# Kernel optimization log

Measured on AMD Instinct MI355X. Metric: run time of the kernel, lower is better.

## Reference

```python
import jax, jax.numpy as jnp
import numpy as np

T, B, V, H = 2048, 32, 512, 512


def setup_inputs() -> dict:
    key = jax.random.key(0)
    ks = jax.random.split(key, 7)
    s = 1.0 / np.sqrt(V + H)  # torch nn.Linear default init bound
    u = lambda k, shape: jax.random.uniform(k, shape, jnp.float32, -s, s)
    return {
        "inputs": jax.random.normal(ks[0], (T, B, V), jnp.float32),
        "state": jnp.zeros((1, B, H), jnp.float32),
        "W_reset": u(ks[1], (V + H, H)),
        "b_reset": u(ks[2], (H,)),
        "W_net": u(ks[3], (V + H, H)),
        "b_net": u(ks[4], (H,)),
        "W_update": u(ks[5], (V + H, H)),
        "b_update": u(ks[6], (H,)),
    }


def reference(inputs, state, W_reset, b_reset, W_net, b_net, W_update, b_update):
    # inputs: [T, B, V], state: [1, B, H]
    h0 = state[0]  # [B, H]

    def step(h, x):
        # x: [B, V], h: [B, H]
        xh = jnp.concatenate([x, h], axis=-1)               # [B, V+H]
        R = jax.nn.sigmoid(xh @ W_reset + b_reset)          # [B, H]
        xr = jnp.concatenate([x, h * R], axis=-1)           # [B, V+H]
        H_t = jnp.tanh(xr @ W_net + b_net)                  # candidate
        Z = jax.nn.sigmoid(xr @ W_update + b_update)        # NOTE: from (x, h*R), faithful to source
        h_new = Z * h + (1.0 - Z) * H_t
        return h_new, h_new

    h_final, states = jax.lax.scan(step, h0, inputs)        # states: [T, B, H]
    return states, h_final[None]                            # ([T,B,H], [1,B,H])
```

## Files before the change

kernel.cpp:

```cpp
#include <hip/hip_runtime.h>
#include <cstdint>
#include <cstddef>

#define T_STEPS 2048
#define BATCH   32
#define VDIM    512
#define HDIM    512
#define SLICES  8
#define COLS    64
#define KPT     64

typedef _Float16 half2v __attribute__((ext_vector_type(2)));
typedef _Float16 half8v __attribute__((ext_vector_type(8)));

__device__ __forceinline__ float dot2h(half2v a, half2v b, float c) {
#if __has_builtin(__builtin_amdgcn_fdot2)
    return __builtin_amdgcn_fdot2(a, b, c, false);
#else
    return fmaf((float)a.x, (float)b.x, fmaf((float)a.y, (float)b.y, c));
#endif
}

__device__ __forceinline__ unsigned long long loadt(const unsigned long long* p) {
    return __hip_atomic_load(p, __ATOMIC_RELAXED, __HIP_MEMORY_SCOPE_AGENT);
}
__device__ __forceinline__ void storet(unsigned long long* p, float v, unsigned tag) {
    unsigned long long x = ((unsigned long long)tag << 32) | (unsigned)__float_as_uint(v);
    __hip_atomic_store(p, x, __ATOMIC_RELAXED, __HIP_MEMORY_SCOPE_AGENT);
}

__global__ __launch_bounds__(256)
void xproj_gemm(const float* __restrict__ X,
                const float* __restrict__ W0, const float* __restrict__ b0,
                const float* __restrict__ W1, const float* __restrict__ b1,
                const float* __restrict__ W2, const float* __restrict__ b2,
                float* __restrict__ xp, int M)
{
    const int g = blockIdx.z;
    const float* W    = (g == 0) ? W0 : (g == 1) ? W1 : W2;
    const float* bias = (g == 0) ? b0 : (g == 1) ? b1 : b2;
    float* out = xp + (size_t)g * M * HDIM;

    __shared__ float As[16][68];
    __shared__ float Bs[16][64];

    const int tid = threadIdx.x;
    const int tx = tid & 15;
    const int ty = tid >> 4;
    const int row0 = blockIdx.y * 64;
    const int n0   = blockIdx.x * 64;

    const int lm = tid >> 2;
    const int lk = (tid & 3) * 4;
    const int bk = tid >> 4;
    const int bn = (tid & 15) * 4;

    float acc[4][4] = {};

    for (int k0 = 0; k0 < VDIM; k0 += 16) {
        float4 av = *(const float4*)&X[(size_t)(row0 + lm) * VDIM + k0 + lk];
        float4 bv = *(const float4*)&W[(size_t)(k0 + bk) * HDIM + n0 + bn];
        __syncthreads();
        As[lk + 0][lm] = av.x;
        As[lk + 1][lm] = av.y;
        As[lk + 2][lm] = av.z;
        As[lk + 3][lm] = av.w;
        *(float4*)&Bs[bk][bn] = bv;
        __syncthreads();
        #pragma unroll
        for (int kk = 0; kk < 16; ++kk) {
            float4 a = *(const float4*)&As[kk][ty * 4];
            float4 b = *(const float4*)&Bs[kk][tx * 4];
            float ar[4] = {a.x, a.y, a.z, a.w};
            float br[4] = {b.x, b.y, b.z, b.w};
            #pragma unroll
            for (int i = 0; i < 4; ++i)
                #pragma unroll
                for (int j = 0; j < 4; ++j)
                    acc[i][j] += ar[i] * br[j];
        }
    }

    float4 bb = *(const float4*)&bias[n0 + tx * 4];
    #pragma unroll
    for (int i = 0; i < 4; ++i) {
        const int row = row0 + ty * 4 + i;
        float4 o;
        o.x = acc[i][0] + bb.x;
        o.y = acc[i][1] + bb.y;
        o.z = acc[i][2] + bb.z;
        o.w = acc[i][3] + bb.w;
        *(float4*)&out[(size_t)row * HDIM + n0 + tx * 4] = o;
    }
}

__global__ __launch_bounds__(512)
__attribute__((amdgpu_waves_per_eu(2, 2)))
void gru_scan3(const float* __restrict__ xp,
               const float* __restrict__ Wrh, const float* __restrict__ Wnh,
               const float* __restrict__ Wzh,
               const float* __restrict__ state, float* __restrict__ out,
               unsigned long long* __restrict__ hT,
               unsigned long long* __restrict__ uT,
               int t0, int nt, int M)
{
    const int b   = blockIdx.x & (BATCH - 1);
    const int s   = blockIdx.x >> 5;
    const int tid = threadIdx.x;
    const int c   = tid & (COLS - 1);
    const int j   = tid >> 6;
    const int n   = s * COLS + c;

    __shared__ __align__(16) _Float16 hlds[HDIM];
    __shared__ __align__(16) _Float16 ulds[HDIM];
    __shared__ float redR[SLICES][COLS];
    __shared__ float redN[SLICES][COLS];
    __shared__ float redZ[SLICES][COLS];

    half2v w2r[KPT / 2], w2n[KPT / 2], w2z[KPT / 2];
    {
        const size_t coloff = (size_t)s * COLS + c;
        const float* pr = Wrh + (size_t)j * KPT * HDIM + coloff;
        const float* pn = Wnh + (size_t)j * KPT * HDIM + coloff;
        const float* pz = Wzh + (size_t)j * KPT * HDIM + coloff;
        #pragma unroll
        for (int q = 0; q < KPT / 2; ++q) {
            half2v r, nn, z;
            r.x  = (_Float16)pr[(size_t)(2 * q) * HDIM];
            r.y  = (_Float16)pr[(size_t)(2 * q + 1) * HDIM];
            nn.x = (_Float16)pn[(size_t)(2 * q) * HDIM];
            nn.y = (_Float16)pn[(size_t)(2 * q + 1) * HDIM];
            z.x  = (_Float16)pz[(size_t)(2 * q) * HDIM];
            z.y  = (_Float16)pz[(size_t)(2 * q + 1) * HDIM];
            w2r[q] = r; w2n[q] = nn; w2z[q] = z;
        }
        #pragma unroll
        for (int q = 0; q < KPT / 2; ++q)
            asm volatile("" : "+v"(w2r[q]), "+v"(w2n[q]), "+v"(w2z[q]));
    }

    const size_t bb32 = (size_t)b * HDIM;
    unsigned long long* hTb = hT + bb32;
    unsigned long long* uTb = uT + bb32;
    const size_t gs = (size_t)M * HDIM;

    for (int tt = 0; tt < nt; ++tt) {
        const int t = t0 + tt;

        float xr = 0.f, xnn = 0.f, xz = 0.f;
        const size_t rb = ((size_t)tt * BATCH + b) * HDIM;
        if (tid < COLS) {
            xr  = xp[rb + n];
            xnn = xp[gs + rb + n];
            xz  = xp[2 * gs + rb + n];
        }

        float hv, hcv = 0.f;
        if (t == 0) {
            hv = state[bb32 + tid];
            if (tid < COLS) hcv = state[bb32 + n];
        } else {
            unsigned long long v;
            do { v = loadt(hTb + tid); } while ((unsigned)(v >> 32) != (unsigned)t);
            hv = __uint_as_float((unsigned)v);
            if (tid < COLS) {
                do { v = loadt(hTb + n); } while ((unsigned)(v >> 32) != (unsigned)t);
                hcv = __uint_as_float((unsigned)v);
            }
        }

        hlds[tid] = (_Float16)hv;
        asm volatile("s_waitcnt lgkmcnt(0)" ::: "memory");
        __builtin_amdgcn_sched_barrier(0);

        {
            float aR = 0.f;
            const half8v* hp = (const half8v*)&hlds[j * KPT];
            #pragma unroll
            for (int q = 0; q < KPT / 8; ++q) {
                half8v h8 = hp[q];
                half2v p0 = {h8[0], h8[1]}, p1 = {h8[2], h8[3]};
                half2v p2 = {h8[4], h8[5]}, p3 = {h8[6], h8[7]};
                aR = dot2h(p0, w2r[4 * q + 0], aR);
                aR = dot2h(p1, w2r[4 * q + 1], aR);
                aR = dot2h(p2, w2r[4 * q + 2], aR);
                aR = dot2h(p3, w2r[4 * q + 3], aR);
            }
            redR[j][c] = aR;
        }
        __syncthreads();

        if (tid < COLS) {
            float sR = 0.f;
            #pragma unroll
            for (int jj = 0; jj < SLICES; ++jj) sR += redR[jj][c];
            float R = 1.f / (1.f + __expf(-(xr + sR)));
            storet(uTb + n, hcv * R, (unsigned)(t + 1));
        }

        {
            unsigned long long v;
            do { v = loadt(uTb + tid); } while ((unsigned)(v >> 32) != (unsigned)(t + 1));
            ulds[tid] = (_Float16)__uint_as_float((unsigned)v);
        }
        asm volatile("s_waitcnt lgkmcnt(0)" ::: "memory");
        __builtin_amdgcn_sched_barrier(0);

        {
            float aN = 0.f, aZ = 0.f;
            const half8v* up = (const half8v*)&ulds[j * KPT];
            #pragma unroll
            for (int q = 0; q < KPT / 8; ++q) {
                half8v u8 = up[q];
                half2v p0 = {u8[0], u8[1]}, p1 = {u8[2], u8[3]};
                half2v p2 = {u8[4], u8[5]}, p3 = {u8[6], u8[7]};
                aN = dot2h(p0, w2n[4 * q + 0], aN);
                aZ = dot2h(p0, w2z[4 * q + 0], aZ);
                aN = dot2h(p1, w2n[4 * q + 1], aN);
                aZ = dot2h(p1, w2z[4 * q + 1], aZ);
                aN = dot2h(p2, w2n[4 * q + 2], aN);
                aZ = dot2h(p2, w2z[4 * q + 2], aZ);
                aN = dot2h(p3, w2n[4 * q + 3], aN);
                aZ = dot2h(p3, w2z[4 * q + 3], aZ);
            }
            redN[j][c] = aN;
            redZ[j][c] = aZ;
        }
        __syncthreads();

        if (tid < COLS) {
            float sN = 0.f, sZ = 0.f;
            #pragma unroll
            for (int jj = 0; jj < SLICES; ++jj) { sN += redN[jj][c]; sZ += redZ[jj][c]; }
            float e  = __expf(2.f * (xnn + sN));
            float Hc = 1.f - 2.f / (e + 1.f);
            float Z  = 1.f / (1.f + __expf(-(xz + sZ)));
            float hnew = Z * hcv + (1.f - Z) * Hc;
            __builtin_nontemporal_store(hnew, out + (size_t)t * BATCH * HDIM + bb32 + n);
            storet(hTb + n, hnew, (unsigned)(t + 1));
            if (t == T_STEPS - 1)
                out[(size_t)T_STEPS * BATCH * HDIM + bb32 + n] = hnew;
        }
    }
}

extern "C" void kernel_launch(void* const* d_in, const int* in_sizes, int n_in,
                              void* d_out, int out_size, void* d_ws, size_t ws_size,
                              hipStream_t stream) {
    const float* inputs   = (const float*)d_in[0];
    const float* state    = (const float*)d_in[1];
    const float* W_reset  = (const float*)d_in[2];
    const float* b_reset  = (const float*)d_in[3];
    const float* W_net    = (const float*)d_in[4];
    const float* b_net    = (const float*)d_in[5];
    const float* W_update = (const float*)d_in[6];
    const float* b_update = (const float*)d_in[7];
    float* out = (float*)d_out;

    const size_t tail_bytes = 2ull * BATCH * HDIM * 8;
    size_t tail_base = (ws_size - tail_bytes) & ~(size_t)255;
    char* base = (char*)d_ws;
    float* xp = (float*)base;
    unsigned long long* hT = (unsigned long long*)(base + tail_base);
    unsigned long long* uT = hT + (size_t)BATCH * HDIM;

    const size_t per_t = 3ull * BATCH * HDIM * sizeof(float);
    int C = (int)(tail_base / per_t);
    if (C > T_STEPS) C = T_STEPS;
    C &= ~1;
    if (C < 2) C = 2;

    hipMemsetAsync(hT, 0xFF, tail_bytes, stream);

    for (int t0 = 0; t0 < T_STEPS; t0 += C) {
        const int nt = (T_STEPS - t0 < C) ? (T_STEPS - t0) : C;
        const int M  = nt * BATCH;

        dim3 g1(HDIM / 64, M / 64, 3);
        xproj_gemm<<<g1, 256, 0, stream>>>(inputs + (size_t)t0 * BATCH * VDIM,
                                           W_reset, b_reset,
                                           W_net,   b_net,
                                           W_update, b_update,
                                           xp, M);

        gru_scan3<<<BATCH * SLICES, 512, 0, stream>>>(
            xp,
            W_reset  + (size_t)VDIM * HDIM,
            W_net    + (size_t)VDIM * HDIM,
            W_update + (size_t)VDIM * HDIM,
            state, out, hT, uT, t0, nt, M);
    }
}
```

Before: 6.490 ms.

## Add fast sc0 flag path with slow atomic fallback for cross-block handoff

The tagged h and u values are now published twice: once with a raw sc0 global store into a 'fast' buffer and once with the agent-scope atomic store into a 'slow' buffer. Pollers read the fast buffer twice with inline-asm sc0 loads before falling back to the atomic load. The goal is lower latency for the per-step inter-workgroup handoff, which bounds the sequential recurrence. The owned column's h (hcv) is also kept in a register across steps instead of being re-polled each step, and the h publish is moved ahead of the output store. In exchange, visibility of the fast path depends on cache-coherence behaviour of sc0 on MI355X, every publish issues an extra store, and the workspace tail doubles in size.

Result: slower. 7.297 ms (+12.4%).

```diff
diff --git a/kernel.cpp b/kernel.cpp
--- a/kernel.cpp
+++ b/kernel.cpp
@@ -24,9 +24,33 @@
 __device__ __forceinline__ unsigned long long loadt(const unsigned long long* p) {
     return __hip_atomic_load(p, __ATOMIC_RELAXED, __HIP_MEMORY_SCOPE_AGENT);
 }
-__device__ __forceinline__ void storet(unsigned long long* p, float v, unsigned tag) {
+__device__ __forceinline__ unsigned long long fload(const unsigned long long* p) {
+    unsigned long long r;
+    asm volatile("global_load_dwordx2 %0, %1, off sc0\n\ts_waitcnt vmcnt(0)"
+                 : "=v"(r) : "v"(p) : "memory");
+    return r;
+}
+__device__ __forceinline__ void fstore(unsigned long long* p, unsigned long long x) {
+    asm volatile("global_store_dwordx2 %0, %1, off sc0" :: "v"(p), "v"(x) : "memory");
+}
+
+__device__ __forceinline__ void publish(unsigned long long* fast, unsigned long long* slow,
+                                        float v, unsigned tag) {
     unsigned long long x = ((unsigned long long)tag << 32) | (unsigned)__float_as_uint(v);
-    __hip_atomic_store(p, x, __ATOMIC_RELAXED, __HIP_MEMORY_SCOPE_AGENT);
+    fstore(fast, x);
+    __hip_atomic_store(slow, x, __ATOMIC_RELAXED, __HIP_MEMORY_SCOPE_AGENT);
+}
+
+__device__ __forceinline__ float poll_tag(const unsigned long long* fast,
+                                          const unsigned long long* slow, unsigned want) {
+    for (;;) {
+        unsigned long long v = fload(fast);
+        if ((unsigned)(v >> 32) == want) return __uint_as_float((unsigned)v);
+        v = fload(fast);
+        if ((unsigned)(v >> 32) == want) return __uint_as_float((unsigned)v);
+        v = loadt(slow);
+        if ((unsigned)(v >> 32) == want) return __uint_as_float((unsigned)v);
+    }
 }
 
 __global__ __launch_bounds__(256)
@@ -96,12 +120,12 @@
 
 __global__ __launch_bounds__(512)
 __attribute__((amdgpu_waves_per_eu(2, 2)))
-void gru_scan3(const float* __restrict__ xp,
+void gru_scan4(const float* __restrict__ xp,
                const float* __restrict__ Wrh, const float* __restrict__ Wnh,
                const float* __restrict__ Wzh,
                const float* __restrict__ state, float* __restrict__ out,
-               unsigned long long* __restrict__ hT,
-               unsigned long long* __restrict__ uT,
+               unsigned long long* __restrict__ hS, unsigned long long* __restrict__ uS,
+               unsigned long long* __restrict__ hF, unsigned long long* __restrict__ uF,
                int t0, int nt, int M)
 {
     const int b   = blockIdx.x & (BATCH - 1);
@@ -140,9 +164,13 @@
     }
 
     const size_t bb32 = (size_t)b * HDIM;
-    unsigned long long* hTb = hT + bb32;
-    unsigned long long* uTb = uT + bb32;
+    unsigned long long* hSb = hS + bb32;
+    unsigned long long* uSb = uS + bb32;
+    unsigned long long* hFb = hF + bb32;
+    unsigned long long* uFb = uF + bb32;
     const size_t gs = (size_t)M * HDIM;
+
+    float hcv = 0.f;
 
     for (int tt = 0; tt < nt; ++tt) {
         const int t = t0 + tt;
@@ -155,18 +183,14 @@
             xz  = xp[2 * gs + rb + n];
         }
 
-        float hv, hcv = 0.f;
+        float hv;
         if (t == 0) {
             hv = state[bb32 + tid];
             if (tid < COLS) hcv = state[bb32 + n];
         } else {
-            unsigned long long v;
-            do { v = loadt(hTb + tid); } while ((unsigned)(v >> 32) != (unsigned)t);
-            hv = __uint_as_float((unsigned)v);
-            if (tid < COLS) {
-                do { v = loadt(hTb + n); } while ((unsigned)(v >> 32) != (unsigned)t);
-                hcv = __uint_as_float((unsigned)v);
-            }
+            hv = poll_tag(hFb + tid, hSb + tid, (unsigned)t);
+            if (tt == 0 && tid < COLS)
+                hcv = poll_tag(hFb + n, hSb + n, (unsigned)t);
         }
 
         hlds[tid] = (_Float16)hv;
@@ -195,14 +219,10 @@
             #pragma unroll
             for (int jj = 0; jj < SLICES; ++jj) sR += redR[jj][c];
             float R = 1.f / (1.f + __expf(-(xr + sR)));
-            storet(uTb + n, hcv * R, (unsigned)(t + 1));
-        }
-
-        {
-            unsigned long long v;
-            do { v = loadt(uTb + tid); } while ((unsigned)(v >> 32) != (unsigned)(t + 1));
-            ulds[tid] = (_Float16)__uint_as_float((unsigned)v);
-        }
+            publish(uFb + n, uSb + n, hcv * R, (unsigned)(t + 1));
+        }
+
+        ulds[tid] = (_Float16)poll_tag(uFb + tid, uSb + tid, (unsigned)(t + 1));
         asm volatile("s_waitcnt lgkmcnt(0)" ::: "memory");
         __builtin_amdgcn_sched_barrier(0);
 
@@ -236,8 +256,9 @@
             float Hc = 1.f - 2.f / (e + 1.f);
             float Z  = 1.f / (1.f + __expf(-(xz + sZ)));
             float hnew = Z * hcv + (1.f - Z) * Hc;
+            publish(hFb + n, hSb + n, hnew, (unsigned)(t + 1));
             __builtin_nontemporal_store(hnew, out + (size_t)t * BATCH * HDIM + bb32 + n);
-            storet(hTb + n, hnew, (unsigned)(t + 1));
+            hcv = hnew;
             if (t == T_STEPS - 1)
                 out[(size_t)T_STEPS * BATCH * HDIM + bb32 + n] = hnew;
         }
@@ -257,12 +278,15 @@
     const float* b_update = (const float*)d_in[7];
     float* out = (float*)d_out;
 
-    const size_t tail_bytes = 2ull * BATCH * HDIM * 8;
+    const size_t buf_elems = (size_t)BATCH * HDIM;
+    const size_t tail_bytes = 4ull * buf_elems * 8;
     size_t tail_base = (ws_size - tail_bytes) & ~(size_t)255;
     char* base = (char*)d_ws;
     float* xp = (float*)base;
-    unsigned long long* hT = (unsigned long long*)(base + tail_base);
-    unsigned long long* uT = hT + (size_t)BATCH * HDIM;
+    unsigned long long* hS = (unsigned long long*)(base + tail_base);
+    unsigned long long* uS = hS + buf_elems;
+    unsigned long long* hF = uS + buf_elems;
+    unsigned long long* uF = hF + buf_elems;
 
     const size_t per_t = 3ull * BATCH * HDIM * sizeof(float);
     int C = (int)(tail_base / per_t);
@@ -270,7 +294,7 @@
     C &= ~1;
     if (C < 2) C = 2;
 
-    hipMemsetAsync(hT, 0xFF, tail_bytes, stream);
+    hipMemsetAsync(hS, 0xFF, tail_bytes, stream);
 
     for (int t0 = 0; t0 < T_STEPS; t0 += C) {
         const int nt = (T_STEPS - t0 < C) ? (T_STEPS - t0) : C;
@@ -283,11 +307,11 @@
                                            W_update, b_update,
                                            xp, M);
 
-        gru_scan3<<<BATCH * SLICES, 512, 0, stream>>>(
+        gru_scan4<<<BATCH * SLICES, 512, 0, stream>>>(
             xp,
             W_reset  + (size_t)VDIM * HDIM,
             W_net    + (size_t)VDIM * HDIM,
             W_update + (size_t)VDIM * HDIM,
-            state, out, hT, uT, t0, nt, M);
-    }
-}
+            state, out, hS, uS, hF, uF, t0, nt, M);
+    }
+}
```

## Repartition recurrent GEMVs by K-slice and exchange tagged partial sums instead of h

Applied to the files above, without the earlier changes.

The N and Z weight matrices are now split by input rows: each block owns a 64-row slice of h*R and computes partial sums for all 512 output columns. Each block keeps the full hidden state locally and exchanges tagged partial-sum packets (N in fp32, Z in fp16) through double-buffered global slots. This removes the cross-block h broadcast and the u exchange, leaving one global exchange per step instead of two. The cost is that every block redundantly computes the full h update, and each thread now polls eight global slots every step. Z partials are rounded to fp16 before being summed.

Measured after the change: 7.870 ms. 21.3% more time.

```diff
diff --git a/kernel.cpp b/kernel.cpp
--- a/kernel.cpp
+++ b/kernel.cpp
@@ -8,7 +8,6 @@
 #define HDIM    512
 #define SLICES  8
 #define COLS    64
-#define KPT     64
 
 typedef _Float16 half2v __attribute__((ext_vector_type(2)));
 typedef _Float16 half8v __attribute__((ext_vector_type(8)));
@@ -24,8 +23,7 @@
 __device__ __forceinline__ unsigned long long loadt(const unsigned long long* p) {
     return __hip_atomic_load(p, __ATOMIC_RELAXED, __HIP_MEMORY_SCOPE_AGENT);
 }
-__device__ __forceinline__ void storet(unsigned long long* p, float v, unsigned tag) {
-    unsigned long long x = ((unsigned long long)tag << 32) | (unsigned)__float_as_uint(v);
+__device__ __forceinline__ void storet(unsigned long long* p, unsigned long long x) {
     __hip_atomic_store(p, x, __ATOMIC_RELAXED, __HIP_MEMORY_SCOPE_AGENT);
 }
 
@@ -96,12 +94,12 @@
 
 __global__ __launch_bounds__(512)
 __attribute__((amdgpu_waves_per_eu(2, 2)))
-void gru_scan3(const float* __restrict__ xp,
+void gru_scan5(const float* __restrict__ xp,
                const float* __restrict__ Wrh, const float* __restrict__ Wnh,
                const float* __restrict__ Wzh,
                const float* __restrict__ state, float* __restrict__ out,
-               unsigned long long* __restrict__ hT,
-               unsigned long long* __restrict__ uT,
+               unsigned long long* __restrict__ part,
+               unsigned long long* __restrict__ hC,
                int t0, int nt, int M)
 {
     const int b   = blockIdx.x & (BATCH - 1);
@@ -109,22 +107,18 @@
     const int tid = threadIdx.x;
     const int c   = tid & (COLS - 1);
     const int j   = tid >> 6;
-    const int n   = s * COLS + c;
 
     __shared__ __align__(16) _Float16 hlds[HDIM];
-    __shared__ __align__(16) _Float16 ulds[HDIM];
+    __shared__ __align__(16) _Float16 ulds[COLS];
     __shared__ float redR[SLICES][COLS];
-    __shared__ float redN[SLICES][COLS];
-    __shared__ float redZ[SLICES][COLS];
-
-    half2v w2r[KPT / 2], w2n[KPT / 2], w2z[KPT / 2];
+
+    half2v w2r[32], w2n[32], w2z[32];
     {
-        const size_t coloff = (size_t)s * COLS + c;
-        const float* pr = Wrh + (size_t)j * KPT * HDIM + coloff;
-        const float* pn = Wnh + (size_t)j * KPT * HDIM + coloff;
-        const float* pz = Wzh + (size_t)j * KPT * HDIM + coloff;
+        const float* pr = Wrh + (size_t)(j * 64) * HDIM + (s * COLS + c);
+        const float* pn = Wnh + (size_t)(s * 64) * HDIM + tid;
+        const float* pz = Wzh + (size_t)(s * 64) * HDIM + tid;
         #pragma unroll
-        for (int q = 0; q < KPT / 2; ++q) {
+        for (int q = 0; q < 32; ++q) {
             half2v r, nn, z;
             r.x  = (_Float16)pr[(size_t)(2 * q) * HDIM];
             r.y  = (_Float16)pr[(size_t)(2 * q + 1) * HDIM];
@@ -135,49 +129,42 @@
             w2r[q] = r; w2n[q] = nn; w2z[q] = z;
         }
         #pragma unroll
-        for (int q = 0; q < KPT / 2; ++q)
+        for (int q = 0; q < 32; ++q)
             asm volatile("" : "+v"(w2r[q]), "+v"(w2n[q]), "+v"(w2z[q]));
     }
 
-    const size_t bb32 = (size_t)b * HDIM;
-    unsigned long long* hTb = hT + bb32;
-    unsigned long long* uTb = uT + bb32;
+    const size_t bb = (size_t)b * HDIM;
     const size_t gs = (size_t)M * HDIM;
+    const size_t pstride = (size_t)BATCH * HDIM;
+
+    float hreg;
+    if (t0 == 0) {
+        hreg = state[bb + tid];
+    } else {
+        unsigned long long v = loadt(hC + bb + tid);
+        while ((unsigned)(v & 0xFFFFu) != (unsigned)(t0 & 0xFFFF))
+            v = loadt(hC + bb + tid);
+        hreg = __uint_as_float((unsigned)(v >> 32));
+    }
+    hlds[tid] = (_Float16)hreg;
+    __syncthreads();
 
     for (int tt = 0; tt < nt; ++tt) {
         const int t = t0 + tt;
-
-        float xr = 0.f, xnn = 0.f, xz = 0.f;
+        const int p = t & 1;
+        const unsigned want = (unsigned)((t + 1) & 0xFFFF);
+
         const size_t rb = ((size_t)tt * BATCH + b) * HDIM;
-        if (tid < COLS) {
-            xr  = xp[rb + n];
-            xnn = xp[gs + rb + n];
-            xz  = xp[2 * gs + rb + n];
-        }
-
-        float hv, hcv = 0.f;
-        if (t == 0) {
-            hv = state[bb32 + tid];
-            if (tid < COLS) hcv = state[bb32 + n];
-        } else {
-            unsigned long long v;
-            do { v = loadt(hTb + tid); } while ((unsigned)(v >> 32) != (unsigned)t);
-            hv = __uint_as_float((unsigned)v);
-            if (tid < COLS) {
-                do { v = loadt(hTb + n); } while ((unsigned)(v >> 32) != (unsigned)t);
-                hcv = __uint_as_float((unsigned)v);
-            }
-        }
-
-        hlds[tid] = (_Float16)hv;
-        asm volatile("s_waitcnt lgkmcnt(0)" ::: "memory");
-        __builtin_amdgcn_sched_barrier(0);
+        float xr = 0.f;
+        if (j == s) xr = xp[rb + tid];
+        const float xnn = xp[gs + rb + tid];
+        const float xz  = xp[2 * gs + rb + tid];
 
         {
             float aR = 0.f;
-            const half8v* hp = (const half8v*)&hlds[j * KPT];
-            #pragma unroll
-            for (int q = 0; q < KPT / 8; ++q) {
+            const half8v* hp = (const half8v*)&hlds[j * 64];
+            #pragma unroll
+            for (int q = 0; q < 8; ++q) {
                 half8v h8 = hp[q];
                 half2v p0 = {h8[0], h8[1]}, p1 = {h8[2], h8[3]};
                 half2v p2 = {h8[4], h8[5]}, p3 = {h8[6], h8[7]};
@@ -190,27 +177,20 @@
         }
         __syncthreads();
 
-        if (tid < COLS) {
+        if (j == s) {
             float sR = 0.f;
             #pragma unroll
             for (int jj = 0; jj < SLICES; ++jj) sR += redR[jj][c];
             float R = 1.f / (1.f + __expf(-(xr + sR)));
-            storet(uTb + n, hcv * R, (unsigned)(t + 1));
-        }
-
-        {
-            unsigned long long v;
-            do { v = loadt(uTb + tid); } while ((unsigned)(v >> 32) != (unsigned)(t + 1));
-            ulds[tid] = (_Float16)__uint_as_float((unsigned)v);
-        }
-        asm volatile("s_waitcnt lgkmcnt(0)" ::: "memory");
-        __builtin_amdgcn_sched_barrier(0);
+            ulds[c] = (_Float16)(hreg * R);
+        }
+        __syncthreads();
 
         {
             float aN = 0.f, aZ = 0.f;
-            const half8v* up = (const half8v*)&ulds[j * KPT];
-            #pragma unroll
-            for (int q = 0; q < KPT / 8; ++q) {
+            const half8v* up = (const half8v*)ulds;
+            #pragma unroll
+            for (int q = 0; q < 8; ++q) {
                 half8v u8 = up[q];
                 half2v p0 = {u8[0], u8[1]}, p1 = {u8[2], u8[3]};
                 half2v p2 = {u8[4], u8[5]}, p3 = {u8[6], u8[7]};
@@ -223,24 +203,50 @@
                 aN = dot2h(p3, w2n[4 * q + 3], aN);
                 aZ = dot2h(p3, w2z[4 * q + 3], aZ);
             }
-            redN[j][c] = aN;
-            redZ[j][c] = aZ;
-        }
-        __syncthreads();
-
-        if (tid < COLS) {
+            union { unsigned short u; _Float16 h; } zc; zc.h = (_Float16)aZ;
+            unsigned long long pkt = ((unsigned long long)__float_as_uint(aN) << 32)
+                                   | ((unsigned long long)zc.u << 16) | want;
+            storet(part + ((size_t)p * SLICES + s) * pstride + bb + tid, pkt);
+        }
+
+        unsigned long long pk[SLICES];
+        {
+            unsigned long long* pbase = part + (size_t)p * SLICES * pstride + bb + tid;
+            #pragma unroll
+            for (int ss = 0; ss < SLICES; ++ss)
+                pk[ss] = loadt(pbase + (size_t)ss * pstride);
+            #pragma unroll
+            for (int ss = 0; ss < SLICES; ++ss)
+                while ((unsigned)(pk[ss] & 0xFFFFu) != want)
+                    pk[ss] = loadt(pbase + (size_t)ss * pstride);
+        }
+
+        {
             float sN = 0.f, sZ = 0.f;
             #pragma unroll
-            for (int jj = 0; jj < SLICES; ++jj) { sN += redN[jj][c]; sZ += redZ[jj][c]; }
+            for (int ss = 0; ss < SLICES; ++ss) {
+                sN += __uint_as_float((unsigned)(pk[ss] >> 32));
+                union { unsigned short u; _Float16 h; } zc;
+                zc.u = (unsigned short)(pk[ss] >> 16);
+                sZ += (float)zc.h;
+            }
             float e  = __expf(2.f * (xnn + sN));
             float Hc = 1.f - 2.f / (e + 1.f);
             float Z  = 1.f / (1.f + __expf(-(xz + sZ)));
-            float hnew = Z * hcv + (1.f - Z) * Hc;
-            __builtin_nontemporal_store(hnew, out + (size_t)t * BATCH * HDIM + bb32 + n);
-            storet(hTb + n, hnew, (unsigned)(t + 1));
-            if (t == T_STEPS - 1)
-                out[(size_t)T_STEPS * BATCH * HDIM + bb32 + n] = hnew;
-        }
+            float hnew = Z * hreg + (1.f - Z) * Hc;
+            hreg = hnew;
+            hlds[tid] = (_Float16)hnew;
+
+            if (j == s) {
+                __builtin_nontemporal_store(hnew, out + (size_t)t * BATCH * HDIM + bb + tid);
+                if (t == T_STEPS - 1)
+                    out[(size_t)T_STEPS * BATCH * HDIM + bb + tid] = hnew;
+                if (tt == nt - 1)
+                    storet(hC + bb + tid,
+                           ((unsigned long long)__float_as_uint(hnew) << 32) | want);
+            }
+        }
+        __syncthreads();
     }
 }
 
@@ -257,12 +263,14 @@
     const float* b_update = (const float*)d_in[7];
     float* out = (float*)d_out;
 
-    const size_t tail_bytes = 2ull * BATCH * HDIM * 8;
+    const size_t buf_elems  = (size_t)BATCH * HDIM;
+    const size_t part_elems = 2ull * SLICES * buf_elems;
+    const size_t tail_bytes = (part_elems + buf_elems) * 8;
     size_t tail_base = (ws_size - tail_bytes) & ~(size_t)255;
     char* base = (char*)d_ws;
     float* xp = (float*)base;
-    unsigned long long* hT = (unsigned long long*)(base + tail_base);
-    unsigned long long* uT = hT + (size_t)BATCH * HDIM;
+    unsigned long long* part = (unsigned long long*)(base + tail_base);
+    unsigned long long* hC   = part + part_elems;
 
     const size_t per_t = 3ull * BATCH * HDIM * sizeof(float);
     int C = (int)(tail_base / per_t);
@@ -270,7 +278,7 @@
     C &= ~1;
     if (C < 2) C = 2;
 
-    hipMemsetAsync(hT, 0xFF, tail_bytes, stream);
+    hipMemsetAsync(part, 0xFF, tail_bytes, stream);
 
     for (int t0 = 0; t0 < T_STEPS; t0 += C) {
         const int nt = (T_STEPS - t0 < C) ? (T_STEPS - t0) : C;
@@ -283,11 +291,11 @@
                                            W_update, b_update,
                                            xp, M);
 
-        gru_scan3<<<BATCH * SLICES, 512, 0, stream>>>(
+        gru_scan5<<<BATCH * SLICES, 512, 0, stream>>>(
             xp,
             W_reset  + (size_t)VDIM * HDIM,
             W_net    + (size_t)VDIM * HDIM,
             W_update + (size_t)VDIM * HDIM,
-            state, out, hT, uT, t0, nt, M);
-    }
-}
+            state, out, part, hC, t0, nt, M);
+    }
+}
```

## Replace FP32 SIMT input-projection GEMM with FP16 MFMA kernel

Applied to the files above, without the earlier changes.

Rewrites the precomputed input-projection GEMM to use 16x16x32 FP16 MFMA instructions. Each block now stages a 512x64 weight slice in LDS as half precision and streams X rows directly from global memory, converting them to FP16 on the fly. The grid is remapped to 128-row tiles, and the chunk size is rounded to a multiple of four so the tiles divide evenly. This targets the FP32 FMA cost of the projection at the price of reduced input precision and uncoalesced strided weight loads during staging.

Result: faster. 5.461 ms (-15.9%).

```diff
diff --git a/kernel.cpp b/kernel.cpp
--- a/kernel.cpp
+++ b/kernel.cpp
@@ -9,9 +9,12 @@
 #define SLICES  8
 #define COLS    64
 #define KPT     64
+#define BM      128
+#define BN      64
 
 typedef _Float16 half2v __attribute__((ext_vector_type(2)));
 typedef _Float16 half8v __attribute__((ext_vector_type(8)));
+typedef float    f32x4  __attribute__((ext_vector_type(4)));
 
 __device__ __forceinline__ float dot2h(half2v a, half2v b, float c) {
 #if __has_builtin(__builtin_amdgcn_fdot2)
@@ -30,67 +33,74 @@
 }
 
 __global__ __launch_bounds__(256)
-void xproj_gemm(const float* __restrict__ X,
+void xproj_mfma(const float* __restrict__ X,
                 const float* __restrict__ W0, const float* __restrict__ b0,
                 const float* __restrict__ W1, const float* __restrict__ b1,
                 const float* __restrict__ W2, const float* __restrict__ b2,
                 float* __restrict__ xp, int M)
 {
-    const int g = blockIdx.z;
+    const int g  = blockIdx.x >> 3;
+    const int n0 = (blockIdx.x & 7) * BN;
+    const int m0 = blockIdx.y * BM;
     const float* W    = (g == 0) ? W0 : (g == 1) ? W1 : W2;
     const float* bias = (g == 0) ? b0 : (g == 1) ? b1 : b2;
     float* out = xp + (size_t)g * M * HDIM;
 
-    __shared__ float As[16][68];
-    __shared__ float Bs[16][64];
-
-    const int tid = threadIdx.x;
-    const int tx = tid & 15;
-    const int ty = tid >> 4;
-    const int row0 = blockIdx.y * 64;
-    const int n0   = blockIdx.x * 64;
-
-    const int lm = tid >> 2;
-    const int lk = (tid & 3) * 4;
-    const int bk = tid >> 4;
-    const int bn = (tid & 15) * 4;
-
-    float acc[4][4] = {};
-
-    for (int k0 = 0; k0 < VDIM; k0 += 16) {
-        float4 av = *(const float4*)&X[(size_t)(row0 + lm) * VDIM + k0 + lk];
-        float4 bv = *(const float4*)&W[(size_t)(k0 + bk) * HDIM + n0 + bn];
-        __syncthreads();
-        As[lk + 0][lm] = av.x;
-        As[lk + 1][lm] = av.y;
-        As[lk + 2][lm] = av.z;
-        As[lk + 3][lm] = av.w;
-        *(float4*)&Bs[bk][bn] = bv;
-        __syncthreads();
-        #pragma unroll
-        for (int kk = 0; kk < 16; ++kk) {
-            float4 a = *(const float4*)&As[kk][ty * 4];
-            float4 b = *(const float4*)&Bs[kk][tx * 4];
-            float ar[4] = {a.x, a.y, a.z, a.w};
-            float br[4] = {b.x, b.y, b.z, b.w};
-            #pragma unroll
-            for (int i = 0; i < 4; ++i)
-                #pragma unroll
-                for (int j = 0; j < 4; ++j)
-                    acc[i][j] += ar[i] * br[j];
-        }
-    }
-
-    float4 bb = *(const float4*)&bias[n0 + tx * 4];
+    __shared__ __align__(16) _Float16 Blds[64 * 64 * 8];
+
+    const int tid  = threadIdx.x;
+    const int lane = tid & 63;
+    const int w    = tid >> 6;
+    const int r16  = lane & 15;
+    const int kq   = lane >> 4;
+
+    {
+        const int c = tid & 63;
+        #pragma unroll
+        for (int it = 0; it < 16; ++it) {
+            const int kg = (tid >> 6) + 4 * it;
+            const float* src = W + (size_t)(kg * 8) * HDIM + n0 + c;
+            half8v v;
+            #pragma unroll
+            for (int i = 0; i < 8; ++i) v[i] = (_Float16)src[(size_t)i * HDIM];
+            *(half8v*)&Blds[(size_t)(kg * 64 + c) * 8] = v;
+        }
+    }
+    __syncthreads();
+
+    f32x4 acc[2][4] = {};
+
+    for (int ks = 0; ks < 16; ++ks) {
+        const int kg = 4 * ks + kq;
+        half8v a[2];
+        #pragma unroll
+        for (int ms = 0; ms < 2; ++ms) {
+            const float* ap = X + (size_t)(m0 + 32 * w + 16 * ms + r16) * VDIM + kg * 8;
+            float4 a0 = *(const float4*)ap;
+            float4 a1 = *(const float4*)(ap + 4);
+            a[ms][0] = (_Float16)a0.x; a[ms][1] = (_Float16)a0.y;
+            a[ms][2] = (_Float16)a0.z; a[ms][3] = (_Float16)a0.w;
+            a[ms][4] = (_Float16)a1.x; a[ms][5] = (_Float16)a1.y;
+            a[ms][6] = (_Float16)a1.z; a[ms][7] = (_Float16)a1.w;
+        }
+        #pragma unroll
+        for (int cb = 0; cb < 4; ++cb) {
+            half8v bf = *(const half8v*)&Blds[(size_t)(kg * 64 + 16 * cb + r16) * 8];
+            acc[0][cb] = __builtin_amdgcn_mfma_f32_16x16x32_f16(a[0], bf, acc[0][cb], 0, 0, 0);
+            acc[1][cb] = __builtin_amdgcn_mfma_f32_16x16x32_f16(a[1], bf, acc[1][cb], 0, 0, 0);
+        }
+    }
+
     #pragma unroll
-    for (int i = 0; i < 4; ++i) {
-        const int row = row0 + ty * 4 + i;
-        float4 o;
-        o.x = acc[i][0] + bb.x;
-        o.y = acc[i][1] + bb.y;
-        o.z = acc[i][2] + bb.z;
-        o.w = acc[i][3] + bb.w;
-        *(float4*)&out[(size_t)row * HDIM + n0 + tx * 4] = o;
+    for (int cb = 0; cb < 4; ++cb) {
+        const float bb = bias[n0 + 16 * cb + r16];
+        #pragma unroll
+        for (int ms = 0; ms < 2; ++ms)
+            #pragma unroll
+            for (int r = 0; r < 4; ++r) {
+                const int row = m0 + 32 * w + 16 * ms + 4 * kq + r;
+                out[(size_t)row * HDIM + n0 + 16 * cb + r16] = acc[ms][cb][r] + bb;
+            }
     }
 }
 
@@ -267,8 +277,8 @@
     const size_t per_t = 3ull * BATCH * HDIM * sizeof(float);
     int C = (int)(tail_base / per_t);
     if (C > T_STEPS) C = T_STEPS;
-    C &= ~1;
-    if (C < 2) C = 2;
+    C &= ~3;
+    if (C < 4) C = 4;
 
     hipMemsetAsync(hT, 0xFF, tail_bytes, stream);
 
@@ -276,8 +286,8 @@
         const int nt = (T_STEPS - t0 < C) ? (T_STEPS - t0) : C;
         const int M  = nt * BATCH;
 
-        dim3 g1(HDIM / 64, M / 64, 3);
-        xproj_gemm<<<g1, 256, 0, stream>>>(inputs + (size_t)t0 * BATCH * VDIM,
+        dim3 g1(8 * 3, M / BM);
+        xproj_mfma<<<g1, 256, 0, stream>>>(inputs + (size_t)t0 * BATCH * VDIM,
                                            W_reset, b_reset,
                                            W_net,   b_net,
                                            W_update, b_update,
```
